# Kernel tuning notes

Hardware: AMD Instinct MI355X
Metric: run time of the kernel (lower is better)

Reference implementation:

```python
import jax, jax.numpy as jnp
import numpy as np

B, L, IN_DIM = 4, 2048, 1024
H, D = 16, 64
OUT_DIM = 1024


def setup_inputs() -> dict:
    key = jax.random.key(0)
    k1, k2, k3 = jax.random.split(key, 3)
    inputs = jax.random.normal(k1, (B, L, IN_DIM), dtype=jnp.float32)
    # nn.Linear weight init scale ~ 1/sqrt(fan_in); keep values moderate
    W_qkv = jax.random.normal(k2, (IN_DIM, 3 * H * D), dtype=jnp.float32) * (IN_DIM ** -0.5)
    W_out = jax.random.normal(k3, (H * D, OUT_DIM), dtype=jnp.float32) * ((H * D) ** -0.5)
    return {"inputs": inputs, "W_qkv": W_qkv, "W_out": W_out}


def reference(inputs, W_qkv, W_out):
    b, l, _ = inputs.shape
    qkv = inputs @ W_qkv                      # [B, L, 3*H*D]
    q, k, v = jnp.split(qkv, 3, axis=-1)
    q = q.reshape(b, l, H, D)
    k = k.reshape(b, l, H, D)
    v = v.reshape(b, l, H, D)
    score = jnp.einsum('bihd,bjhd->bijh', q, k) / (D ** 0.5)  # [B, L, L, H]
    # sequence_mask(arange(1..L)) == lower-triangular causal mask
    mask = jnp.tril(jnp.ones((l, l), dtype=score.dtype))[None, :, :, None]
    masked_score = score * mask + 1e30 * (mask - 1.0)
    wmat = jax.nn.softmax(masked_score, axis=2)
    out = jnp.einsum('bijh,bjhd->bihd', wmat, v).reshape(b, l, H * D)
    return out @ W_out
```

## Files before the change

kernel.cpp:

```cpp
#include <hip/hip_runtime.h>

#define DEVI __device__ __forceinline__

typedef __attribute__((ext_vector_type(8))) short bh8;
typedef __attribute__((ext_vector_type(4))) float f32x4;

static constexpr int Bsz  = 4;
static constexpr int Lseq = 2048;
static constexpr int INDIM = 1024;
static constexpr int NH = 16;
static constexpr int HD = 64;
static constexpr int QKVN = 3 * NH * HD;
static constexpr int OUTD = 1024;
static constexpr int Mrows = Bsz * Lseq;

DEVI unsigned short f2bf(float f) {
    unsigned u = __float_as_uint(f);
    u = u + 0x7fffu + ((u >> 16) & 1u);
    return (unsigned short)(u >> 16);
}

DEVI void gl2lds16(const unsigned short* g, unsigned short* l) {
    __builtin_amdgcn_global_load_lds(
        (const __attribute__((address_space(1))) void*)g,
        (__attribute__((address_space(3))) void*)l, 16, 0, 0);
}

__global__ __launch_bounds__(256) void convert_f32_bf16(
    const float* __restrict__ in, unsigned short* __restrict__ out, int n8) {
    int i = blockIdx.x * 256 + threadIdx.x;
    if (i >= n8) return;
    const f32x4* p = (const f32x4*)(in + (size_t)i * 8);
    f32x4 a = p[0], b = p[1];
    bh8 o;
    o[0] = (short)f2bf(a[0]); o[1] = (short)f2bf(a[1]);
    o[2] = (short)f2bf(a[2]); o[3] = (short)f2bf(a[3]);
    o[4] = (short)f2bf(b[0]); o[5] = (short)f2bf(b[1]);
    o[6] = (short)f2bf(b[2]); o[7] = (short)f2bf(b[3]);
    *(bh8*)(out + (size_t)i * 8) = o;
}

__global__ __launch_bounds__(256) void transpose_f32_bf16(
    const float* __restrict__ W, unsigned short* __restrict__ Wt, int K, int N) {
    __shared__ unsigned short t[64][65];
    int n0 = blockIdx.x * 64, k0 = blockIdx.y * 64;
    int tid = threadIdx.x;
#pragma unroll
    for (int i = 0; i < 16; ++i) {
        int idx = tid + i * 256;
        int r = idx >> 6, c = idx & 63;
        t[r][c] = f2bf(W[(size_t)(k0 + r) * N + (n0 + c)]);
    }
    __syncthreads();
#pragma unroll
    for (int i = 0; i < 16; ++i) {
        int idx = tid + i * 256;
        int r = idx >> 6, c = idx & 63;
        Wt[(size_t)(n0 + r) * K + (k0 + c)] = t[c][r];
    }
}

template <int MODE>
__global__ __launch_bounds__(256) void gemm_bt(
    const unsigned short* __restrict__ A, const unsigned short* __restrict__ Bt,
    float* __restrict__ Cf, unsigned short* __restrict__ Qg,
    unsigned short* __restrict__ Kg, unsigned short* __restrict__ Vg,
    int K, int ntn) {
    __shared__ unsigned short Al[2][128 * 32];
    __shared__ unsigned short Bl[2][128 * 32];
    int tid = threadIdx.x;
    int lane = tid & 63, wave = tid >> 6;
    int mt = blockIdx.x / ntn, nt_ = blockIdx.x % ntn;
    int m0 = mt * 128, n0 = nt_ * 128;
    int wm = (wave >> 1) * 64, wn = (wave & 1) * 64;

    int srow = tid >> 2;
    int skof = (tid & 3) * 8;
    const unsigned short* Ags = A + (size_t)(m0 + srow) * K + skof;
    const unsigned short* Bgs = Bt + (size_t)(n0 + srow) * K + skof;
    int wofs = wave * 512;

    f32x4 acc[4][4] = {};
    int cl = lane & 15, kq = (lane >> 4) * 8;

    int nt = K >> 5;
    gl2lds16(Ags, &Al[0][0] + wofs);
    gl2lds16(Ags + (size_t)64 * K, &Al[0][0] + 2048 + wofs);
    gl2lds16(Bgs, &Bl[0][0] + wofs);
    gl2lds16(Bgs + (size_t)64 * K, &Bl[0][0] + 2048 + wofs);
    __syncthreads();

    int cur = 0;
    for (int t = 0; t < nt; ++t) {
        if (t + 1 < nt) {
            int k1 = (t + 1) * 32;
            gl2lds16(Ags + k1, &Al[cur ^ 1][0] + wofs);
            gl2lds16(Ags + (size_t)64 * K + k1, &Al[cur ^ 1][0] + 2048 + wofs);
            gl2lds16(Bgs + k1, &Bl[cur ^ 1][0] + wofs);
            gl2lds16(Bgs + (size_t)64 * K + k1, &Bl[cur ^ 1][0] + 2048 + wofs);
        }
        bh8 af[4], bf[4];
#pragma unroll
        for (int mi = 0; mi < 4; ++mi)
            af[mi] = *(const bh8*)(&Al[cur][0] + (wm + mi * 16 + cl) * 32 + kq);
#pragma unroll
        for (int nj = 0; nj < 4; ++nj)
            bf[nj] = *(const bh8*)(&Bl[cur][0] + (wn + nj * 16 + cl) * 32 + kq);
#pragma unroll
        for (int mi = 0; mi < 4; ++mi)
#pragma unroll
            for (int nj = 0; nj < 4; ++nj)
                acc[mi][nj] = __builtin_amdgcn_mfma_f32_16x16x32_bf16(
                    af[mi], bf[nj], acc[mi][nj], 0, 0, 0);
        if (t + 1 < nt) __syncthreads();
        cur ^= 1;
    }

    int rb = (lane >> 4) * 4;
#pragma unroll
    for (int mi = 0; mi < 4; ++mi) {
#pragma unroll
        for (int nj = 0; nj < 4; ++nj) {
#pragma unroll
            for (int r = 0; r < 4; ++r) {
                int gm = m0 + wm + mi * 16 + rb + r;
                int gn = n0 + wn + nj * 16 + cl;
                float v = acc[mi][nj][r];
                if (MODE == 0) {
                    int b = gm >> 11, ls = gm & 2047;
                    int sel = gn >> 10, h = (gn >> 6) & 15, d = gn & 63;
                    if (sel == 0)
                        Qg[((size_t)(b * NH + h) * Lseq + ls) * HD + d] = f2bf(v * 0.125f);
                    else if (sel == 1)
                        Kg[((size_t)(b * NH + h) * Lseq + ls) * HD + d] = f2bf(v);
                    else
                        Vg[((size_t)(b * NH + h) * HD + d) * Lseq + ls] = f2bf(v);
                } else {
                    Cf[(size_t)gm * OUTD + gn] = v;
                }
            }
        }
    }
}

__global__ __launch_bounds__(256) void attn_causal(
    const unsigned short* __restrict__ Qg, const unsigned short* __restrict__ Kg,
    const unsigned short* __restrict__ Vt, unsigned short* __restrict__ Og) {
    __shared__ unsigned short Kl[64 * 64];
    __shared__ unsigned short Vl[64 * 64];
    __shared__ unsigned short Pl[4][16 * 72];
    int tid = threadIdx.x, wave = tid >> 6, lane = tid & 63;
    int bid = blockIdx.x;
    int xcd = bid & 7, slot = bid >> 3;
    int p = slot & 15;
    int bh = ((slot >> 4) << 3) | xcd;
    int b = bh >> 4, h = bh & 15;
    const unsigned short* Qp = Qg + (size_t)bh * Lseq * HD;
    const unsigned short* Kp = Kg + (size_t)bh * Lseq * HD;
    const unsigned short* Vp = Vt + (size_t)bh * HD * Lseq;
    int cl = lane & 15, kq = (lane >> 4) * 8, rb = (lane >> 4) * 4;
    unsigned short* Pw = &Pl[wave][0];

    int srow = tid >> 2;
    int sc0 = (tid & 3) * 16;
    int ssw = (srow & 7) << 3;

    bh8 ones;
#pragma unroll
    for (int i = 0; i < 8; ++i) ones[i] = (short)0x3F80;

    for (int pass = 0; pass < 2; ++pass) {
        int pt = pass ? (31 - p) : p;
        int q0 = pt * 64 + wave * 16;

        bh8 qf0 = *(const bh8*)(Qp + (size_t)(q0 + cl) * HD + kq);
        bh8 qf1 = *(const bh8*)(Qp + (size_t)(q0 + cl) * HD + 32 + kq);

        f32x4 o[4] = {};
        f32x4 osum = {};

        int nblk = pt + 1;
        for (int j = 0; j < nblk; ++j) {
            int kv0 = j * 64;
            const unsigned short* Ks = Kp + (size_t)(kv0 + srow) * HD;
            const unsigned short* Vs = Vp + (size_t)srow * Lseq + kv0;
            bh8 k0 = *(const bh8*)(Ks + sc0);
            bh8 k1 = *(const bh8*)(Ks + sc0 + 8);
            bh8 v0 = *(const bh8*)(Vs + sc0);
            bh8 v1 = *(const bh8*)(Vs + sc0 + 8);
            __syncthreads();
            *(bh8*)(Kl + srow * 64 + (sc0 ^ ssw)) = k0;
            *(bh8*)(Kl + srow * 64 + ((sc0 + 8) ^ ssw)) = k1;
            *(bh8*)(Vl + srow * 64 + (sc0 ^ ssw)) = v0;
            *(bh8*)(Vl + srow * 64 + ((sc0 + 8) ^ ssw)) = v1;
            __syncthreads();
#pragma unroll
            for (int nb = 0; nb < 4; ++nb) {
                int row = nb * 16 + cl, rs = (row & 7) << 3;
                bh8 kf0 = *(const bh8*)(Kl + row * 64 + (kq ^ rs));
                bh8 kf1 = *(const bh8*)(Kl + row * 64 + ((kq + 32) ^ rs));
                f32x4 s = {};
                s = __builtin_amdgcn_mfma_f32_16x16x32_bf16(qf0, kf0, s, 0, 0, 0);
                s = __builtin_amdgcn_mfma_f32_16x16x32_bf16(qf1, kf1, s, 0, 0, 0);
                int col = kv0 + nb * 16 + cl;
#pragma unroll
                for (int r = 0; r < 4; ++r) {
                    float v = s[r];
                    if (col > q0 + rb + r) v = -3e30f;
                    Pw[(rb + r) * 72 + nb * 16 + cl] = f2bf(__expf(v));
                }
            }
            bh8 pa0 = *(const bh8*)(Pw + cl * 72 + kq);
            bh8 pa1 = *(const bh8*)(Pw + cl * 72 + 32 + kq);
#pragma unroll
            for (int db = 0; db < 4; ++db) {
                int dr = db * 16 + cl, ds = (dr & 7) << 3;
                bh8 vf0 = *(const bh8*)(Vl + dr * 64 + (kq ^ ds));
                bh8 vf1 = *(const bh8*)(Vl + dr * 64 + ((kq + 32) ^ ds));
                o[db] = __builtin_amdgcn_mfma_f32_16x16x32_bf16(pa0, vf0, o[db], 0, 0, 0);
                o[db] = __builtin_amdgcn_mfma_f32_16x16x32_bf16(pa1, vf1, o[db], 0, 0, 0);
            }
            osum = __builtin_amdgcn_mfma_f32_16x16x32_bf16(pa0, ones, osum, 0, 0, 0);
            osum = __builtin_amdgcn_mfma_f32_16x16x32_bf16(pa1, ones, osum, 0, 0, 0);
        }
#pragma unroll
        for (int r = 0; r < 4; ++r) {
            float inv = 1.0f / osum[r];
            int row = q0 + rb + r;
            size_t obase = (size_t)(b * Lseq + row) * OUTD + h * HD;
#pragma unroll
            for (int db = 0; db < 4; ++db)
                Og[obase + db * 16 + cl] = f2bf(o[db][r] * inv);
        }
    }
}

extern "C" void kernel_launch(void* const* d_in, const int* in_sizes, int n_in,
                              void* d_out, int out_size, void* d_ws, size_t ws_size,
                              hipStream_t stream) {
    (void)in_sizes; (void)n_in; (void)out_size; (void)ws_size;
    const float* X    = (const float*)d_in[0];
    const float* Wqkv = (const float*)d_in[1];
    const float* Wout = (const float*)d_in[2];
    float* out = (float*)d_out;

    char* ws = (char*)d_ws;
    size_t off = 0;
    unsigned short* Xb    = (unsigned short*)(ws + off); off += (size_t)Mrows * INDIM * 2;
    unsigned short* WqkvT = (unsigned short*)(ws + off); off += (size_t)QKVN * INDIM * 2;
    unsigned short* WoutT = (unsigned short*)(ws + off); off += (size_t)OUTD * (NH * HD) * 2;
    unsigned short* Qg    = (unsigned short*)(ws + off); off += (size_t)Mrows * NH * HD * 2;
    unsigned short* Kg    = (unsigned short*)(ws + off); off += (size_t)Mrows * NH * HD * 2;
    unsigned short* Vtg   = (unsigned short*)(ws + off); off += (size_t)Mrows * NH * HD * 2;
    unsigned short* Ob    = (unsigned short*)(ws + off); off += (size_t)Mrows * NH * HD * 2;

    convert_f32_bf16<<<(Mrows * INDIM / 8 + 255) / 256, 256, 0, stream>>>(
        X, Xb, Mrows * INDIM / 8);
    transpose_f32_bf16<<<dim3(QKVN / 64, INDIM / 64), 256, 0, stream>>>(
        Wqkv, WqkvT, INDIM, QKVN);
    transpose_f32_bf16<<<dim3(OUTD / 64, (NH * HD) / 64), 256, 0, stream>>>(
        Wout, WoutT, NH * HD, OUTD);
    gemm_bt<0><<<(Mrows / 128) * (QKVN / 128), 256, 0, stream>>>(
        Xb, WqkvT, nullptr, Qg, Kg, Vtg, INDIM, QKVN / 128);
    attn_causal<<<Bsz * NH * 16, 256, 0, stream>>>(Qg, Kg, Vtg, Ob);
    gemm_bt<1><<<(Mrows / 128) * (OUTD / 128), 256, 0, stream>>>(
        Ob, WoutT, out, nullptr, nullptr, nullptr, NH * HD, OUTD / 128);
}
```

Baseline: 209.5 us.

## Replace QKV projection GEMM with 256x256 tile, 8-phase pipelined kernel

```diff
diff --git a/kernel.cpp b/kernel.cpp
--- a/kernel.cpp
+++ b/kernel.cpp
@@ -57,6 +57,127 @@
         int idx = tid + i * 256;
         int r = idx >> 6, c = idx & 63;
         Wt[(size_t)(n0 + r) * K + (k0 + c)] = t[c][r];
+    }
+}
+
+template <int MODE>
+__global__ __launch_bounds__(512, 2) void gemm256_8ph(
+    const unsigned short* __restrict__ A, const unsigned short* __restrict__ Bt,
+    float* __restrict__ Cf, unsigned short* __restrict__ Qg,
+    unsigned short* __restrict__ Kg, unsigned short* __restrict__ Vg,
+    int ntn, int cpx) {
+    __shared__ unsigned short LA[2][16384];
+    __shared__ unsigned short LB[2][16384];
+    constexpr int K = 1024;
+    int tid = threadIdx.x, lane = tid & 63, wave = tid >> 6;
+    int bid = blockIdx.x;
+    int swz = (bid & 7) * cpx + (bid >> 3);
+    int mt = swz / ntn, nt = swz % ntn;
+    int m0 = mt * 256, n0 = nt * 256;
+    int wr = wave >> 2, wc = wave & 3;
+    int cl = lane & 15, kq = (lane >> 4) * 8;
+
+    int srow = tid >> 3, scol = (tid & 7) * 8;
+    const unsigned short* Ag = A + (size_t)(m0 + srow) * K + scol;
+    const unsigned short* Bg = Bt + (size_t)(n0 + srow) * K + scol;
+    int ldsw = wave * 512;
+
+    auto stA = [&](int t, int hf) {
+        unsigned short* l = &LA[t & 1][hf * 8192] + ldsw;
+        const unsigned short* g = Ag + (size_t)(hf * 128) * K + t * 64;
+        gl2lds16(g, l);
+        gl2lds16(g + (size_t)64 * K, l + 4096);
+    };
+    auto stB = [&](int t, int hf) {
+        unsigned short* l = &LB[t & 1][hf * 8192] + ldsw;
+        const unsigned short* g = Bg + (size_t)(hf * 128) * K + t * 64;
+        gl2lds16(g, l);
+        gl2lds16(g + (size_t)64 * K, l + 4096);
+    };
+
+    f32x4 acc[8][4] = {};
+    bh8 bfr[4][2];
+
+    stA(0, 0); stA(0, 1); stB(0, 0); stB(0, 1); stB(1, 0); stB(1, 1);
+    asm volatile("s_waitcnt vmcnt(4)" ::: "memory");
+    __builtin_amdgcn_s_barrier();
+
+#define PHASE(Q, BUF, ISSUE, WAITV)                                            \
+    {                                                                          \
+        const unsigned short* Ald = &LA[BUF][0];                               \
+        const unsigned short* Bld = &LB[BUF][0];                               \
+        if (Q == 0) {                                                          \
+            _Pragma("unroll")                                                  \
+            for (int nf = 0; nf < 4; ++nf)                                     \
+                _Pragma("unroll")                                              \
+                for (int ks = 0; ks < 2; ++ks)                                 \
+                    bfr[nf][ks] = *(const bh8*)(Bld +                          \
+                        (wc * 64 + nf * 16 + cl) * 64 + ks * 32 + kq);         \
+        }                                                                      \
+        bh8 afr[2][2];                                                         \
+        _Pragma("unroll")                                                      \
+        for (int f = 0; f < 2; ++f)                                            \
+            _Pragma("unroll")                                                  \
+            for (int ks = 0; ks < 2; ++ks)                                     \
+                afr[f][ks] = *(const bh8*)(Ald +                               \
+                    (wr * 128 + Q * 32 + f * 16 + cl) * 64 + ks * 32 + kq);    \
+        ISSUE;                                                                 \
+        __builtin_amdgcn_s_barrier();                                          \
+        __builtin_amdgcn_s_setprio(1);                                         \
+        _Pragma("unroll")                                                      \
+        for (int f = 0; f < 2; ++f)                                            \
+            _Pragma("unroll")                                                  \
+            for (int nf = 0; nf < 4; ++nf)                                     \
+                _Pragma("unroll")                                              \
+                for (int ks = 0; ks < 2; ++ks)                                 \
+                    acc[Q * 2 + f][nf] = __builtin_amdgcn_mfma_f32_16x16x32_bf16( \
+                        afr[f][ks], bfr[nf][ks], acc[Q * 2 + f][nf], 0, 0, 0); \
+        __builtin_amdgcn_s_setprio(0);                                         \
+        WAITV;                                                                 \
+        __builtin_amdgcn_s_barrier();                                          \
+    }
+
+    for (int it = 0; it < 8; ++it) {
+        int T = 2 * it;
+        bool n2 = (T + 2) < 16, n3 = (T + 3) < 16;
+        PHASE(0, 0, { stA(T + 1, 0); }, {})
+        PHASE(1, 0, { stA(T + 1, 1); }, {})
+        PHASE(2, 0, { if (n2) stB(T + 2, 0); }, {})
+        PHASE(3, 0, { if (n2) stB(T + 2, 1); },
+              { if (n2) asm volatile("s_waitcnt vmcnt(4)" ::: "memory");
+                else    asm volatile("s_waitcnt vmcnt(0)" ::: "memory"); })
+        PHASE(0, 1, { if (n2) stA(T + 2, 0); }, {})
+        PHASE(1, 1, { if (n2) stA(T + 2, 1); }, {})
+        PHASE(2, 1, { if (n3) stB(T + 3, 0); }, {})
+        PHASE(3, 1, { if (n3) stB(T + 3, 1); },
+              { if (n3) asm volatile("s_waitcnt vmcnt(4)" ::: "memory"); })
+    }
+#undef PHASE
+
+    int rb = (lane >> 4) * 4;
+#pragma unroll
+    for (int mi = 0; mi < 8; ++mi) {
+#pragma unroll
+        for (int nj = 0; nj < 4; ++nj) {
+#pragma unroll
+            for (int r = 0; r < 4; ++r) {
+                int gm = m0 + wr * 128 + mi * 16 + rb + r;
+                int gn = n0 + wc * 64 + nj * 16 + cl;
+                float v = acc[mi][nj][r];
+                if (MODE == 0) {
+                    int b = gm >> 11, ls = gm & 2047;
+                    int sel = gn >> 10, h = (gn >> 6) & 15, d = gn & 63;
+                    if (sel == 0)
+                        Qg[((size_t)(b * NH + h) * Lseq + ls) * HD + d] = f2bf(v * 0.125f);
+                    else if (sel == 1)
+                        Kg[((size_t)(b * NH + h) * Lseq + ls) * HD + d] = f2bf(v);
+                    else
+                        Vg[((size_t)(b * NH + h) * HD + d) * Lseq + ls] = f2bf(v);
+                } else {
+                    Cf[(size_t)gm * OUTD + gn] = v;
+                }
+            }
+        }
     }
 }
 
@@ -260,8 +381,8 @@
         Wqkv, WqkvT, INDIM, QKVN);
     transpose_f32_bf16<<<dim3(OUTD / 64, (NH * HD) / 64), 256, 0, stream>>>(
         Wout, WoutT, NH * HD, OUTD);
-    gemm_bt<0><<<(Mrows / 128) * (QKVN / 128), 256, 0, stream>>>(
-        Xb, WqkvT, nullptr, Qg, Kg, Vtg, INDIM, QKVN / 128);
+    gemm256_8ph<0><<<(Mrows / 256) * (QKVN / 256), 512, 0, stream>>>(
+        Xb, WqkvT, nullptr, Qg, Kg, Vtg, QKVN / 256, (Mrows / 256) * (QKVN / 256) / 8);
     attn_causal<<<Bsz * NH * 16, 256, 0, stream>>>(Qg, Kg, Vtg, Ob);
     gemm_bt<1><<<(Mrows / 128) * (OUTD / 128), 256, 0, stream>>>(
         Ob, WoutT, out, nullptr, nullptr, nullptr, NH * HD, OUTD / 128);
```

Measured after the change: 233.8 us. +11.6%, slower.
